# Kernel tuning notes

Measured on AMD Instinct MI355X. Metric: run time of the kernel, lower is better.

## Reference

```python
import jax, jax.numpy as jnp
import numpy as np

NUM_HEADS = 16
HIDDEN = 1024
HEAD_DIM = HIDDEN // NUM_HEADS


def setup_inputs() -> dict:
    key = jax.random.key(0)
    ks = jax.random.split(key, 9)
    B, S, D = 2, 2048, HIDDEN
    s = 1.0 / np.sqrt(D)
    return {
        "x": jax.random.normal(ks[0], (B, S, D), dtype=jnp.float32),
        "Wq": jax.random.normal(ks[1], (D, D), dtype=jnp.float32) * s,
        "bq": jnp.zeros((D,), dtype=jnp.float32),
        "Wk": jax.random.normal(ks[2], (D, D), dtype=jnp.float32) * s,
        "bk": jnp.zeros((D,), dtype=jnp.float32),
        "Wv": jax.random.normal(ks[3], (D, D), dtype=jnp.float32) * s,
        "bv": jnp.zeros((D,), dtype=jnp.float32),
        "Wo": jax.random.normal(ks[4], (D, D), dtype=jnp.float32) * s,
        "bo": jnp.zeros((D,), dtype=jnp.float32),
    }


def reference(x, Wq, bq, Wk, bk, Wv, bv, Wo, bo):
    B, S, D = x.shape
    H, Hd = NUM_HEADS, HEAD_DIM
    # projections -> [B, H, S, Hd]
    def proj(W, b):
        return (x @ W + b).reshape(B, S, H, Hd).transpose(0, 2, 1, 3)
    q = proj(Wq, bq)
    k = proj(Wk, bk)
    v = proj(Wv, bv)
    scores = jnp.einsum('bhqd,bhkd->bhqk', q, k) / jnp.sqrt(jnp.float32(Hd))
    p_attn = jax.nn.softmax(scores, axis=-1)  # dropout = identity (eval)
    ctx = jnp.einsum('bhqk,bhkd->bhqd', p_attn, v)
    attn_mean = jnp.mean(p_attn, axis=1)  # [B, S, S]
    out = ctx.transpose(0, 2, 1, 3).reshape(B, S, D) @ Wo + bo
    return out, attn_mean
```

## Files before the change

### kernel.cpp

```cpp
#include <hip/hip_runtime.h>
#include <math.h>

#define NUM_HEADS 16
#define HEAD_DIM  64
#define HIDDEN    1024
#define BATCH     2
#define SEQ       2048

#define QSCALE 0.1803368801111204f

typedef short bf16x8 __attribute__((ext_vector_type(8)));
typedef short short4v __attribute__((ext_vector_type(4)));
typedef float f32x4 __attribute__((ext_vector_type(4)));

#if __has_builtin(__builtin_amdgcn_exp2f)
#define EXP2F __builtin_amdgcn_exp2f
#else
#define EXP2F exp2f
#endif

__device__ __forceinline__ short f2bf(float f) {
    union { float f; unsigned int u; } x; x.f = f;
    unsigned int r = x.u + 0x7fffu + ((x.u >> 16) & 1u);
    return (short)(r >> 16);
}

__device__ __forceinline__ unsigned int pack_bf16_trunc(float lo, float hi) {
    return __builtin_amdgcn_perm(__float_as_uint(hi), __float_as_uint(lo), 0x07060302u);
}

__device__ __forceinline__ void async16(const void* g, void* l) {
    __builtin_amdgcn_global_load_lds(
        (const __attribute__((address_space(1))) void*)g,
        (__attribute__((address_space(3))) void*)l, 16, 0, 0);
}

__global__ __launch_bounds__(256)
void prep_kernel(const float* __restrict__ x,
                 const float* __restrict__ Wq, const float* __restrict__ Wk,
                 const float* __restrict__ Wv, const float* __restrict__ Wo,
                 short* __restrict__ xb, short* __restrict__ Wt4)
{
    __shared__ float t[64][65];
    const int tid = threadIdx.x;
    const int bid = blockIdx.x;
    if (bid < 4096) {
        size_t i = ((size_t)bid * 256 + tid) * 4;
        float4 v = *(const float4*)&x[i];
        short4v o;
        o.x = f2bf(v.x); o.y = f2bf(v.y); o.z = f2bf(v.z); o.w = f2bf(v.w);
        *(short4v*)&xb[i] = o;
        return;
    }
    const int tb = bid - 4096;
    const int z  = tb >> 8;
    const int cx = tb & 15, cy = (tb >> 4) & 15;
    const float* W = (z == 0) ? Wq : (z == 1) ? Wk : (z == 2) ? Wv : Wo;
    short* dst = Wt4 + (size_t)z * HIDDEN * HIDDEN;
    const int c0 = cx * 64;
    const int r0 = cy * 64;
    const int cl = tid & 63, rw = tid >> 6;
    #pragma unroll
    for (int p = 0; p < 16; ++p) {
        int row = p * 4 + rw;
        t[row][cl] = W[(size_t)(r0 + row) * HIDDEN + c0 + cl];
    }
    __syncthreads();
    #pragma unroll
    for (int p = 0; p < 16; ++p) {
        int orow = p * 4 + rw;
        dst[(size_t)(c0 + orow) * HIDDEN + r0 + cl] = f2bf(t[cl][orow]);
    }
}

__global__ __launch_bounds__(256)
void qkv_proj_kernel(const short* __restrict__ xb, const short* __restrict__ Wt4,
                     const float* __restrict__ bq, const float* __restrict__ bk,
                     const float* __restrict__ bv,
                     short* __restrict__ Qb, short* __restrict__ Kb,
                     short* __restrict__ Vt)
{
    __shared__ short ldsA[128 * 32];
    __shared__ short ldsB[128 * 32];
    const int tid = threadIdx.x;
    const int lane = tid & 63, w = tid >> 6;
    const int l = lane & 15, q = lane >> 4;
    const int n0 = blockIdx.x * 128;
    const int m0 = blockIdx.y * 128;
    const int z  = blockIdx.z;
    const short* Wt = Wt4 + (size_t)z * HIDDEN * HIDDEN;
    const int wm = (w >> 1) * 64, wn = (w & 1) * 64;
    const int kc = q ^ ((l >> 1) & 3);

    f32x4 acc[4][4];
    #pragma unroll
    for (int i = 0; i < 4; ++i)
        #pragma unroll
        for (int j = 0; j < 4; ++j)
            acc[i][j] = (f32x4){0.f, 0.f, 0.f, 0.f};

    for (int k0 = 0; k0 < HIDDEN; k0 += 32) {
        #pragma unroll
        for (int half = 0; half < 2; ++half) {
            int c = half * 256 + tid;
            int row = c >> 2;
            int kcg = (c & 3) ^ ((row >> 1) & 3);
            async16(xb + (size_t)(m0 + row) * HIDDEN + k0 + kcg * 8, &ldsA[c * 8]);
            async16(Wt + (size_t)(n0 + row) * HIDDEN + k0 + kcg * 8, &ldsB[c * 8]);
        }
        __syncthreads();
        bf16x8 af[4], bfr[4];
        #pragma unroll
        for (int i = 0; i < 4; ++i)
            af[i] = *(const bf16x8*)&ldsA[((wm + 16 * i + l) * 4 + kc) * 8];
        #pragma unroll
        for (int j = 0; j < 4; ++j)
            bfr[j] = *(const bf16x8*)&ldsB[((wn + 16 * j + l) * 4 + kc) * 8];
        #pragma unroll
        for (int i = 0; i < 4; ++i)
            #pragma unroll
            for (int j = 0; j < 4; ++j)
                acc[i][j] = __builtin_amdgcn_mfma_f32_16x16x32_bf16(
                    af[i], bfr[j], acc[i][j], 0, 0, 0);
        __syncthreads();
    }

    const float* bias = (z == 0) ? bq : (z == 1) ? bk : bv;
    const float sc = (z == 0) ? QSCALE : 1.0f;
    if (z < 2) {
        short* Ob = (z == 0) ? Qb : Kb;
        #pragma unroll
        for (int j = 0; j < 4; ++j) {
            int n = n0 + wn + 16 * j + l;
            float bval = bias[n];
            int h = n >> 6, hd = n & 63;
            #pragma unroll
            for (int i = 0; i < 4; ++i) {
                #pragma unroll
                for (int reg = 0; reg < 4; ++reg) {
                    int m = m0 + wm + 16 * i + 4 * q + reg;
                    int b_ = m >> 11, s = m & 2047;
                    Ob[(((size_t)(b_ * NUM_HEADS + h) * SEQ) + s) * HEAD_DIM + hd] =
                        f2bf((acc[i][j][reg] + bval) * sc);
                }
            }
        }
    } else {
        #pragma unroll
        for (int j = 0; j < 4; ++j) {
            int n = n0 + wn + 16 * j + l;
            float bval = bias[n];
            int h = n >> 6, hd = n & 63;
            #pragma unroll
            for (int i = 0; i < 4; ++i) {
                int mb = m0 + wm + 16 * i + 4 * q;
                int b_ = mb >> 11, s = mb & 2047;
                short4v pk;
                #pragma unroll
                for (int reg = 0; reg < 4; ++reg)
                    pk[reg] = f2bf(acc[i][j][reg] + bval);
                *(short4v*)&Vt[(((size_t)(b_ * NUM_HEADS + h) * HEAD_DIM) + hd) * SEQ + s] = pk;
            }
        }
    }
}

__global__ __launch_bounds__(256)
void out_proj_kernel(const short* __restrict__ Cb, const short* __restrict__ Wot,
                     const float* __restrict__ bo, float* __restrict__ out)
{
    __shared__ short ldsA[64 * 32];
    __shared__ short ldsB[128 * 32];
    const int tid = threadIdx.x;
    const int lane = tid & 63, w = tid >> 6;
    const int l = lane & 15, q = lane >> 4;
    const int n0 = blockIdx.x * 128;
    const int m0 = blockIdx.y * 64;
    const int kc = q ^ ((l >> 1) & 3);

    f32x4 acc[4][2];
    #pragma unroll
    for (int i = 0; i < 4; ++i)
        #pragma unroll
        for (int j = 0; j < 2; ++j)
            acc[i][j] = (f32x4){0.f, 0.f, 0.f, 0.f};

    for (int k0 = 0; k0 < HIDDEN; k0 += 32) {
        const int h = k0 >> 6, hdb = k0 & 63;
        {
            int c = tid;
            int row = c >> 2;
            int kcg = (c & 3) ^ ((row >> 1) & 3);
            int m = m0 + row;
            int b_ = m >> 11, s = m & 2047;
            async16(Cb + (((size_t)(b_ * NUM_HEADS + h) * SEQ) + s) * HEAD_DIM + hdb + kcg * 8,
                    &ldsA[c * 8]);
        }
        #pragma unroll
        for (int half = 0; half < 2; ++half) {
            int c = half * 256 + tid;
            int row = c >> 2;
            int kcg = (c & 3) ^ ((row >> 1) & 3);
            async16(Wot + (size_t)(n0 + row) * HIDDEN + k0 + kcg * 8, &ldsB[c * 8]);
        }
        __syncthreads();
        bf16x8 af[4], bfr[2];
        #pragma unroll
        for (int i = 0; i < 4; ++i)
            af[i] = *(const bf16x8*)&ldsA[((16 * i + l) * 4 + kc) * 8];
        #pragma unroll
        for (int j = 0; j < 2; ++j)
            bfr[j] = *(const bf16x8*)&ldsB[((32 * w + 16 * j + l) * 4 + kc) * 8];
        #pragma unroll
        for (int i = 0; i < 4; ++i)
            #pragma unroll
            for (int j = 0; j < 2; ++j)
                acc[i][j] = __builtin_amdgcn_mfma_f32_16x16x32_bf16(
                    af[i], bfr[j], acc[i][j], 0, 0, 0);
        __syncthreads();
    }

    #pragma unroll
    for (int j = 0; j < 2; ++j) {
        int n = n0 + 32 * w + 16 * j + l;
        float bval = bo[n];
        #pragma unroll
        for (int i = 0; i < 4; ++i)
            #pragma unroll
            for (int reg = 0; reg < 4; ++reg) {
                int m = m0 + 16 * i + 4 * q + reg;
                out[(size_t)m * HIDDEN + n] = acc[i][j][reg] + bval;
            }
    }
}

__global__ __launch_bounds__(256)
void flash_kernel(const short* __restrict__ Qb, const short* __restrict__ Kb,
                  const short* __restrict__ Vt, short* __restrict__ Cb,
                  float* __restrict__ Lb)
{
    __shared__ short Qs[128 * 64];
    __shared__ short Ks[64 * 64];
    __shared__ short Vs[64 * 64];
    __shared__ short Ps[4 * 2 * 16 * 72];

    const int tid = threadIdx.x, lane = tid & 63, w = tid >> 6;
    const int l = lane & 15, q = lane >> 4;
    const int q0 = blockIdx.x * 128;
    const int h = blockIdx.y, b = blockIdx.z;
    const size_t base  = (size_t)(b * NUM_HEADS + h) * SEQ * HEAD_DIM;
    const size_t vbase = (size_t)(b * NUM_HEADS + h) * HEAD_DIM * SEQ;
    short* Pw = &Ps[w * 2304];

    #pragma unroll
    for (int i = 0; i < 4; ++i) {
        int c = 256 * i + tid;
        int row = c >> 3;
        int g = ((c & 7) ^ (row & 7)) * 8;
        async16(Qb + base + (size_t)(q0 + row) * HEAD_DIM + g, &Qs[c * 8]);
    }

    const int c1 = tid, c2 = 256 + tid;
    const int row1 = c1 >> 3, row2 = c2 >> 3;
    const int g1 = ((c1 & 7) ^ (row1 & 7)) * 8;
    const int g2 = ((c2 & 7) ^ (row2 & 7)) * 8;
    const short* kp1 = Kb + base + (size_t)row1 * HEAD_DIM + g1;
    const short* kp2 = Kb + base + (size_t)row2 * HEAD_DIM + g2;
    const short* vp1 = Vt + vbase + (size_t)row1 * SEQ + g1;
    const short* vp2 = Vt + vbase + (size_t)row2 * SEQ + g2;

    f32x4 ctx[2][4];
    #pragma unroll
    for (int u = 0; u < 2; ++u)
        #pragma unroll
        for (int t = 0; t < 4; ++t) ctx[u][t] = (f32x4){0.f, 0.f, 0.f, 0.f};
    float l_part[2] = {0.f, 0.f};

    for (int kt = 0; kt < SEQ; kt += 64) {
        async16(kp1, &Ks[c1 * 8]);
        async16(kp2, &Ks[c2 * 8]);
        async16(vp1, &Vs[c1 * 8]);
        async16(vp2, &Vs[c2 * 8]);
        kp1 += 64 * HEAD_DIM; kp2 += 64 * HEAD_DIM;
        vp1 += 64;            vp2 += 64;
        __syncthreads();

        f32x4 st[2][4];
        #pragma unroll
        for (int u = 0; u < 2; ++u)
            #pragma unroll
            for (int t = 0; t < 4; ++t) st[u][t] = (f32x4){0.f, 0.f, 0.f, 0.f};
        #pragma unroll
        for (int ks = 0; ks < 2; ++ks) {
            int cc = (4 * ks + q) ^ (l & 7);
            bf16x8 bq0 = *(const bf16x8*)&Qs[((32 * w + l) * 8 + cc) * 8];
            bf16x8 bq1 = *(const bf16x8*)&Qs[((32 * w + 16 + l) * 8 + cc) * 8];
            #pragma unroll
            for (int t = 0; t < 4; ++t) {
                bf16x8 ak = *(const bf16x8*)&Ks[((16 * t + l) * 8 + cc) * 8];
                st[0][t] = __builtin_amdgcn_mfma_f32_16x16x32_bf16(ak, bq0, st[0][t], 0, 0, 0);
                st[1][t] = __builtin_amdgcn_mfma_f32_16x16x32_bf16(ak, bq1, st[1][t], 0, 0, 0);
            }
        }

        #pragma unroll
        for (int u = 0; u < 2; ++u) {
            #pragma unroll
            for (int t = 0; t < 4; ++t) {
                float p0 = EXP2F(st[u][t][0]);
                float p1 = EXP2F(st[u][t][1]);
                float p2 = EXP2F(st[u][t][2]);
                float p3 = EXP2F(st[u][t][3]);
                l_part[u] += (p0 + p1) + (p2 + p3);
                uint2 pk;
                pk.x = pack_bf16_trunc(p0, p1);
                pk.y = pack_bf16_trunc(p2, p3);
                *(uint2*)&Pw[u * 1152 + l * 72 + 16 * t + 4 * q] = pk;
            }
        }

        #pragma unroll
        for (int ks = 0; ks < 2; ++ks) {
            int cc = (4 * ks + q) ^ (l & 7);
            bf16x8 bp0 = *(const bf16x8*)&Pw[l * 72 + ks * 32 + q * 8];
            bf16x8 bp1 = *(const bf16x8*)&Pw[1152 + l * 72 + ks * 32 + q * 8];
            #pragma unroll
            for (int t = 0; t < 4; ++t) {
                bf16x8 av = *(const bf16x8*)&Vs[((16 * t + l) * 8 + cc) * 8];
                ctx[0][t] = __builtin_amdgcn_mfma_f32_16x16x32_bf16(av, bp0, ctx[0][t], 0, 0, 0);
                ctx[1][t] = __builtin_amdgcn_mfma_f32_16x16x32_bf16(av, bp1, ctx[1][t], 0, 0, 0);
            }
        }
        __syncthreads();
    }

    #pragma unroll
    for (int u = 0; u < 2; ++u) {
        float rs = l_part[u];
        rs += __shfl_xor(rs, 16);
        rs += __shfl_xor(rs, 32);
        float inv_l = 1.0f / rs;
        int s = q0 + 32 * w + 16 * u + l;
        #pragma unroll
        for (int t = 0; t < 4; ++t) {
            short4v pk;
            #pragma unroll
            for (int reg = 0; reg < 4; ++reg)
                pk[reg] = f2bf(ctx[u][t][reg] * inv_l);
            *(short4v*)&Cb[(((size_t)(b * NUM_HEADS + h) * SEQ) + s) * HEAD_DIM + 16 * t + 4 * q] = pk;
        }
        if (q == 0)
            Lb[(size_t)(b * NUM_HEADS + h) * SEQ + s] = rs;
    }
}

__global__ __launch_bounds__(256)
void attn_mean_kernel(const short* __restrict__ Qb, const short* __restrict__ Kb,
                      const float* __restrict__ Lb, float* __restrict__ amean)
{
    __shared__ short Qs[64 * 64];
    __shared__ short Ks[256 * 64];
    __shared__ float Le[64];
    const int tid = threadIdx.x, lane = tid & 63, w = tid >> 6;
    const int l = lane & 15, q = lane >> 4;
    const int k0 = blockIdx.x * 256;
    const int q0 = blockIdx.y * 64;
    const int b  = blockIdx.z;
    const size_t HSTRIDE = (size_t)SEQ * HEAD_DIM;

    const short* qp[2];
    const short* kp[8];
    {
        const size_t base0 = (size_t)(b * NUM_HEADS) * HSTRIDE;
        #pragma unroll
        for (int i = 0; i < 2; ++i) {
            int c = 256 * i + tid;
            int row = c >> 3;
            int g = ((c & 7) ^ (row & 7)) * 8;
            qp[i] = Qb + base0 + (size_t)(q0 + row) * HEAD_DIM + g;
        }
        #pragma unroll
        for (int i = 0; i < 8; ++i) {
            int c = 256 * i + tid;
            int row = c >> 3;
            int g = ((c & 7) ^ (row & 7)) * 8;
            kp[i] = Kb + base0 + (size_t)(k0 + row) * HEAD_DIM + g;
        }
    }

    f32x4 macc[4][4];
    #pragma unroll
    for (int tk = 0; tk < 4; ++tk)
        #pragma unroll
        for (int tq = 0; tq < 4; ++tq)
            macc[tk][tq] = (f32x4){0.f, 0.f, 0.f, 0.f};

    for (int h = 0; h < NUM_HEADS; ++h) {
        #pragma unroll
        for (int i = 0; i < 2; ++i) { async16(qp[i], &Qs[(256 * i + tid) * 8]); qp[i] += HSTRIDE; }
        #pragma unroll
        for (int i = 0; i < 8; ++i) { async16(kp[i], &Ks[(256 * i + tid) * 8]); kp[i] += HSTRIDE; }
        if (tid < 64)
            Le[tid] = 1.0f / Lb[(size_t)(b * NUM_HEADS + h) * SEQ + q0 + tid];
        __syncthreads();

        bf16x8 bq[4][2];
        #pragma unroll
        for (int tq = 0; tq < 4; ++tq)
            #pragma unroll
            for (int ks = 0; ks < 2; ++ks) {
                int cc = (4 * ks + q) ^ (l & 7);
                bq[tq][ks] = *(const bf16x8*)&Qs[((16 * tq + l) * 8 + cc) * 8];
            }

        #pragma unroll
        for (int tk = 0; tk < 4; ++tk) {
            bf16x8 ak[2];
            #pragma unroll
            for (int ks = 0; ks < 2; ++ks) {
                int cc = (4 * ks + q) ^ (l & 7);
                ak[ks] = *(const bf16x8*)&Ks[((64 * w + 16 * tk + l) * 8 + cc) * 8];
            }
            #pragma unroll
            for (int tq = 0; tq < 4; ++tq) {
                f32x4 st = (f32x4){0.f, 0.f, 0.f, 0.f};
                st = __builtin_amdgcn_mfma_f32_16x16x32_bf16(ak[0], bq[tq][0], st, 0, 0, 0);
                st = __builtin_amdgcn_mfma_f32_16x16x32_bf16(ak[1], bq[tq][1], st, 0, 0, 0);
                float li = Le[16 * tq + l];
                #pragma unroll
                for (int reg = 0; reg < 4; ++reg)
                    macc[tk][tq][reg] += EXP2F(st[reg]) * li;
            }
        }
        __syncthreads();
    }

    const float inv_h = 1.0f / (float)NUM_HEADS;
    #pragma unroll
    for (int tq = 0; tq < 4; ++tq) {
        int row_q = q0 + 16 * tq + l;
        #pragma unroll
        for (int tk = 0; tk < 4; ++tk) {
            int col_k = k0 + 64 * w + 16 * tk + 4 * q;
            f32x4 o;
            #pragma unroll
            for (int reg = 0; reg < 4; ++reg) o[reg] = macc[tk][tq][reg] * inv_h;
            *(f32x4*)&amean[((size_t)b * SEQ + row_q) * SEQ + col_k] = o;
        }
    }
}

extern "C" void kernel_launch(void* const* d_in, const int* in_sizes, int n_in,
                              void* d_out, int out_size, void* d_ws, size_t ws_size,
                              hipStream_t stream)
{
    const float* x  = (const float*)d_in[0];
    const float* Wq = (const float*)d_in[1];
    const float* bq = (const float*)d_in[2];
    const float* Wk = (const float*)d_in[3];
    const float* bk = (const float*)d_in[4];
    const float* Wv = (const float*)d_in[5];
    const float* bv = (const float*)d_in[6];
    const float* Wo = (const float*)d_in[7];
    const float* bo = (const float*)d_in[8];

    float* out   = (float*)d_out;
    float* amean = out + (size_t)BATCH * SEQ * HIDDEN;

    const size_t NELEM = (size_t)BATCH * NUM_HEADS * SEQ * HEAD_DIM;
    short* ws  = (short*)d_ws;
    short* xb  = ws;
    short* Wt4 = xb + NELEM;
    short* Qb  = Wt4 + 4 * (size_t)HIDDEN * HIDDEN;
    short* Kb  = Qb + NELEM;
    short* Vt  = Kb + NELEM;
    short* Cb  = Vt + NELEM;
    float* Lb  = (float*)(Cb + NELEM);

    dim3 blk(256);
    prep_kernel<<<dim3(4096 + 1024), blk, 0, stream>>>(x, Wq, Wk, Wv, Wo, xb, Wt4);
    qkv_proj_kernel<<<dim3(8, 32, 3), blk, 0, stream>>>(xb, Wt4, bq, bk, bv, Qb, Kb, Vt);
    flash_kernel<<<dim3(SEQ / 128, NUM_HEADS, BATCH), blk, 0, stream>>>(Qb, Kb, Vt, Cb, Lb);
    attn_mean_kernel<<<dim3(SEQ / 256, SEQ / 64, BATCH), blk, 0, stream>>>(Qb, Kb, Lb, amean);
    out_proj_kernel<<<dim3(8, 64), blk, 0, stream>>>(Cb, Wt4 + 3 * (size_t)HIDDEN * HIDDEN, bo, out);
}
```

Before: 262.4 us.

## Split flash attention key tiles across two warp halves with register-resident P

```diff
diff --git a/kernel.cpp b/kernel.cpp
--- a/kernel.cpp
+++ b/kernel.cpp
@@ -234,123 +234,144 @@
     }
 }
 
-__global__ __launch_bounds__(256)
+__global__ __launch_bounds__(512, 4)
 void flash_kernel(const short* __restrict__ Qb, const short* __restrict__ Kb,
                   const short* __restrict__ Vt, short* __restrict__ Cb,
                   float* __restrict__ Lb)
 {
-    __shared__ short Qs[128 * 64];
     __shared__ short Ks[64 * 64];
     __shared__ short Vs[64 * 64];
-    __shared__ short Ps[4 * 2 * 16 * 72];
+    __shared__ float Xch[4][64][34];
 
     const int tid = threadIdx.x, lane = tid & 63, w = tid >> 6;
     const int l = lane & 15, q = lane >> 4;
+    const int qg = w & 3;
+    const int kh = w >> 2;
     const int q0 = blockIdx.x * 128;
+    const int Q0 = q0 + qg * 32;
     const int h = blockIdx.y, b = blockIdx.z;
     const size_t base  = (size_t)(b * NUM_HEADS + h) * SEQ * HEAD_DIM;
     const size_t vbase = (size_t)(b * NUM_HEADS + h) * HEAD_DIM * SEQ;
-    short* Pw = &Ps[w * 2304];
-
-    #pragma unroll
-    for (int i = 0; i < 4; ++i) {
-        int c = 256 * i + tid;
-        int row = c >> 3;
-        int g = ((c & 7) ^ (row & 7)) * 8;
-        async16(Qb + base + (size_t)(q0 + row) * HEAD_DIM + g, &Qs[c * 8]);
-    }
-
-    const int c1 = tid, c2 = 256 + tid;
-    const int row1 = c1 >> 3, row2 = c2 >> 3;
-    const int g1 = ((c1 & 7) ^ (row1 & 7)) * 8;
-    const int g2 = ((c2 & 7) ^ (row2 & 7)) * 8;
-    const short* kp1 = Kb + base + (size_t)row1 * HEAD_DIM + g1;
-    const short* kp2 = Kb + base + (size_t)row2 * HEAD_DIM + g2;
-    const short* vp1 = Vt + vbase + (size_t)row1 * SEQ + g1;
-    const short* vp2 = Vt + vbase + (size_t)row2 * SEQ + g2;
+
+    const int c = tid;
+    const int row = c >> 3;
+    const int g = ((c & 7) ^ (row & 7)) * 8;
+    const short* kp = Kb + base + (size_t)row * HEAD_DIM + g;
+    const short* vp = Vt + vbase + (size_t)row * SEQ + g;
+
+    bf16x8 bq[2][2];
+    #pragma unroll
+    for (int u = 0; u < 2; ++u)
+        #pragma unroll
+        for (int ks = 0; ks < 2; ++ks)
+            bq[u][ks] = *(const bf16x8*)(Qb + base +
+                (size_t)(Q0 + 16 * u + l) * HEAD_DIM + 32 * ks + 8 * q);
+
+    const int sw = l & 7;
+    int kaddr[2];
+    #pragma unroll
+    for (int ks = 0; ks < 2; ++ks)
+        kaddr[ks] = (32 * kh + l) * 64 + ((4 * ks + q) ^ sw) * 8;
+    const int vc0 = 4 * kh + (q >> 1);
+    const int vaddr0 = l * 64 + ((vc0      ^ sw) * 8) + 4 * (q & 1);
+    const int vaddr1 = l * 64 + (((vc0 + 2) ^ sw) * 8) + 4 * (q & 1);
 
     f32x4 ctx[2][4];
     #pragma unroll
     for (int u = 0; u < 2; ++u)
         #pragma unroll
-        for (int t = 0; t < 4; ++t) ctx[u][t] = (f32x4){0.f, 0.f, 0.f, 0.f};
+        for (int m = 0; m < 4; ++m) ctx[u][m] = (f32x4){0.f, 0.f, 0.f, 0.f};
     float l_part[2] = {0.f, 0.f};
 
     for (int kt = 0; kt < SEQ; kt += 64) {
-        async16(kp1, &Ks[c1 * 8]);
-        async16(kp2, &Ks[c2 * 8]);
-        async16(vp1, &Vs[c1 * 8]);
-        async16(vp2, &Vs[c2 * 8]);
-        kp1 += 64 * HEAD_DIM; kp2 += 64 * HEAD_DIM;
-        vp1 += 64;            vp2 += 64;
-        __syncthreads();
-
-        f32x4 st[2][4];
+        async16(kp, &Ks[c * 8]);
+        async16(vp, &Vs[c * 8]);
+        kp += 64 * HEAD_DIM;
+        vp += 64;
+        __syncthreads();
+
+        f32x4 st[2][2];
         #pragma unroll
         for (int u = 0; u < 2; ++u)
             #pragma unroll
-            for (int t = 0; t < 4; ++t) st[u][t] = (f32x4){0.f, 0.f, 0.f, 0.f};
+            for (int t = 0; t < 2; ++t) st[u][t] = (f32x4){0.f, 0.f, 0.f, 0.f};
         #pragma unroll
         for (int ks = 0; ks < 2; ++ks) {
-            int cc = (4 * ks + q) ^ (l & 7);
-            bf16x8 bq0 = *(const bf16x8*)&Qs[((32 * w + l) * 8 + cc) * 8];
-            bf16x8 bq1 = *(const bf16x8*)&Qs[((32 * w + 16 + l) * 8 + cc) * 8];
-            #pragma unroll
-            for (int t = 0; t < 4; ++t) {
-                bf16x8 ak = *(const bf16x8*)&Ks[((16 * t + l) * 8 + cc) * 8];
-                st[0][t] = __builtin_amdgcn_mfma_f32_16x16x32_bf16(ak, bq0, st[0][t], 0, 0, 0);
-                st[1][t] = __builtin_amdgcn_mfma_f32_16x16x32_bf16(ak, bq1, st[1][t], 0, 0, 0);
-            }
-        }
-
+            #pragma unroll
+            for (int t = 0; t < 2; ++t) {
+                bf16x8 ak = *(const bf16x8*)&Ks[kaddr[ks] + t * 1024];
+                st[0][t] = __builtin_amdgcn_mfma_f32_16x16x32_bf16(ak, bq[0][ks], st[0][t], 0, 0, 0);
+                st[1][t] = __builtin_amdgcn_mfma_f32_16x16x32_bf16(ak, bq[1][ks], st[1][t], 0, 0, 0);
+            }
+        }
+
+        union { unsigned int u32[4]; bf16x8 v; } bp[2];
         #pragma unroll
         for (int u = 0; u < 2; ++u) {
             #pragma unroll
-            for (int t = 0; t < 4; ++t) {
+            for (int t = 0; t < 2; ++t) {
                 float p0 = EXP2F(st[u][t][0]);
                 float p1 = EXP2F(st[u][t][1]);
                 float p2 = EXP2F(st[u][t][2]);
                 float p3 = EXP2F(st[u][t][3]);
                 l_part[u] += (p0 + p1) + (p2 + p3);
-                uint2 pk;
-                pk.x = pack_bf16_trunc(p0, p1);
-                pk.y = pack_bf16_trunc(p2, p3);
-                *(uint2*)&Pw[u * 1152 + l * 72 + 16 * t + 4 * q] = pk;
-            }
-        }
-
-        #pragma unroll
-        for (int ks = 0; ks < 2; ++ks) {
-            int cc = (4 * ks + q) ^ (l & 7);
-            bf16x8 bp0 = *(const bf16x8*)&Pw[l * 72 + ks * 32 + q * 8];
-            bf16x8 bp1 = *(const bf16x8*)&Pw[1152 + l * 72 + ks * 32 + q * 8];
+                bp[u].u32[2 * t]     = pack_bf16_trunc(p0, p1);
+                bp[u].u32[2 * t + 1] = pack_bf16_trunc(p2, p3);
+            }
+        }
+
+        #pragma unroll
+        for (int m = 0; m < 4; ++m) {
+            short4v g0 = *(const short4v*)&Vs[vaddr0 + m * 1024];
+            short4v g1 = *(const short4v*)&Vs[vaddr1 + m * 1024];
+            bf16x8 av = __builtin_shufflevector(g0, g1, 0, 1, 2, 3, 4, 5, 6, 7);
+            ctx[0][m] = __builtin_amdgcn_mfma_f32_16x16x32_bf16(av, bp[0].v, ctx[0][m], 0, 0, 0);
+            ctx[1][m] = __builtin_amdgcn_mfma_f32_16x16x32_bf16(av, bp[1].v, ctx[1][m], 0, 0, 0);
+        }
+        __syncthreads();
+    }
+
+    if (kh == 1) {
+        float* dst = &Xch[qg][lane][0];
+        #pragma unroll
+        for (int u = 0; u < 2; ++u)
+            #pragma unroll
+            for (int m = 0; m < 4; ++m)
+                #pragma unroll
+                for (int r = 0; r < 4; ++r)
+                    dst[u * 16 + m * 4 + r] = ctx[u][m][r];
+        dst[32] = l_part[0];
+        dst[33] = l_part[1];
+    }
+    __syncthreads();
+    if (kh == 0) {
+        const float* src = &Xch[qg][lane][0];
+        #pragma unroll
+        for (int u = 0; u < 2; ++u)
+            #pragma unroll
+            for (int m = 0; m < 4; ++m)
+                #pragma unroll
+                for (int r = 0; r < 4; ++r)
+                    ctx[u][m][r] += src[u * 16 + m * 4 + r];
+
+        #pragma unroll
+        for (int u = 0; u < 2; ++u) {
+            float rs = l_part[u] + src[32 + u];
+            rs += __shfl_xor(rs, 16);
+            rs += __shfl_xor(rs, 32);
+            float inv_l = 1.0f / rs;
+            int s = Q0 + 16 * u + l;
             #pragma unroll
             for (int t = 0; t < 4; ++t) {
-                bf16x8 av = *(const bf16x8*)&Vs[((16 * t + l) * 8 + cc) * 8];
-                ctx[0][t] = __builtin_amdgcn_mfma_f32_16x16x32_bf16(av, bp0, ctx[0][t], 0, 0, 0);
-                ctx[1][t] = __builtin_amdgcn_mfma_f32_16x16x32_bf16(av, bp1, ctx[1][t], 0, 0, 0);
-            }
-        }
-        __syncthreads();
-    }
-
-    #pragma unroll
-    for (int u = 0; u < 2; ++u) {
-        float rs = l_part[u];
-        rs += __shfl_xor(rs, 16);
-        rs += __shfl_xor(rs, 32);
-        float inv_l = 1.0f / rs;
-        int s = q0 + 32 * w + 16 * u + l;
-        #pragma unroll
-        for (int t = 0; t < 4; ++t) {
-            short4v pk;
-            #pragma unroll
-            for (int reg = 0; reg < 4; ++reg)
-                pk[reg] = f2bf(ctx[u][t][reg] * inv_l);
-            *(short4v*)&Cb[(((size_t)(b * NUM_HEADS + h) * SEQ) + s) * HEAD_DIM + 16 * t + 4 * q] = pk;
-        }
-        if (q == 0)
-            Lb[(size_t)(b * NUM_HEADS + h) * SEQ + s] = rs;
+                short4v pk;
+                #pragma unroll
+                for (int reg = 0; reg < 4; ++reg)
+                    pk[reg] = f2bf(ctx[u][t][reg] * inv_l);
+                *(short4v*)&Cb[(((size_t)(b * NUM_HEADS + h) * SEQ) + s) * HEAD_DIM + 16 * t + 4 * q] = pk;
+            }
+            if (q == 0)
+                Lb[(size_t)(b * NUM_HEADS + h) * SEQ + s] = rs;
+        }
     }
 }
 
@@ -480,7 +501,7 @@
     dim3 blk(256);
     prep_kernel<<<dim3(4096 + 1024), blk, 0, stream>>>(x, Wq, Wk, Wv, Wo, xb, Wt4);
     qkv_proj_kernel<<<dim3(8, 32, 3), blk, 0, stream>>>(xb, Wt4, bq, bk, bv, Qb, Kb, Vt);
-    flash_kernel<<<dim3(SEQ / 128, NUM_HEADS, BATCH), blk, 0, stream>>>(Qb, Kb, Vt, Cb, Lb);
+    flash_kernel<<<dim3(SEQ / 128, NUM_HEADS, BATCH), dim3(512), 0, stream>>>(Qb, Kb, Vt, Cb, Lb);
     attn_mean_kernel<<<dim3(SEQ / 256, SEQ / 64, BATCH), blk, 0, stream>>>(Qb, Kb, Lb, amean);
     out_proj_kernel<<<dim3(8, 64), blk, 0, stream>>>(Cb, Wt4 + 3 * (size_t)HIDDEN * HIDDEN, bo, out);
 }
```

After: 251.4 us. -4.2%, faster.
